# Optimization experiments

Measured on AMD Instinct MI355X. Metric: run time of the kernel, lower is better.

Reference implementation:

```python
import jax, jax.numpy as jnp
import numpy as np

DIM = 512
HEADS = 8
HD = 64
FFN = 2048
WIN = 64            # cantor_local_window; also medium-scale stride
N_LOCAL = 64        # budget 128 * 0.5
N_MED = 38          # budget 128 * 0.3
N_GLOB = 26         # remainder (ratio 0.2)
EPS = 1e-5


def _indices(S):
    # Multi-scale O(n) sampling pattern: per-query key indices [S, K].
    pos = jnp.arange(S)[:, None]
    local = jnp.clip(pos + jnp.arange(N_LOCAL) - N_LOCAL // 2, 0, S - 1)
    med_off = (jnp.arange(N_MED) - N_MED // 2) * WIN
    medium = jnp.clip(pos + med_off, 0, S - 1)
    glob = jnp.linspace(0, S - 1, N_GLOB).astype(jnp.int32)
    glob = jnp.broadcast_to(glob[None, :], (S, N_GLOB))
    return jnp.concatenate([local, medium, glob], axis=1)


def _layernorm(x, g, b):
    mu = jnp.mean(x, axis=-1, keepdims=True)
    var = jnp.mean((x - mu) ** 2, axis=-1, keepdims=True)
    return (x - mu) * jax.lax.rsqrt(var + EPS) * g + b


def _cantor_attention(x, mask, wqkv, bqkv, wo, bo):
    B, S, D = x.shape
    qkv = x @ wqkv + bqkv                      # [B,S,3D]
    q, k, v = jnp.split(qkv, 3, axis=-1)
    heads = lambda t: t.reshape(B, S, HEADS, HD).transpose(0, 2, 1, 3)
    q, k, v = heads(q), heads(k), heads(v)     # [B,H,S,hd]
    idx = _indices(S)                          # [S,K]
    k_g = k[:, :, idx, :]                      # [B,H,S,K,hd]
    v_g = v[:, :, idx, :]
    scores = jnp.einsum('bhsd,bhskd->bhsk', q, k_g) / np.sqrt(HD).astype(np.float32)
    m_g = mask[:, idx]                         # [B,S,K]
    scores = jnp.where(m_g[:, None, :, :], scores, jnp.finfo(scores.dtype).min)
    attn = jax.nn.softmax(scores, axis=-1)
    out = jnp.einsum('bhsk,bhskd->bhsd', attn, v_g)
    out = out.transpose(0, 2, 1, 3).reshape(B, S, D)
    return out @ wo + bo


def setup_inputs() -> dict:
    key = jax.random.key(0)
    ks = jax.random.split(key, 8)
    s = lambda fan: 1.0 / np.sqrt(fan)
    return {
        'x': jax.random.normal(ks[0], (1, 2048, DIM), jnp.float32),
        'attention_mask': jnp.ones((1, 2048), jnp.bool_),
        'ln1_g': jnp.ones((DIM,), jnp.float32),
        'ln1_b': jnp.zeros((DIM,), jnp.float32),
        'ln2_g': jnp.ones((DIM,), jnp.float32),
        'ln2_b': jnp.zeros((DIM,), jnp.float32),
        'wqkv': jax.random.normal(ks[1], (DIM, 3 * DIM), jnp.float32) * s(DIM),
        'bqkv': jnp.zeros((3 * DIM,), jnp.float32),
        'wo': jax.random.normal(ks[2], (DIM, DIM), jnp.float32) * s(DIM),
        'bo': jnp.zeros((DIM,), jnp.float32),
        'w1': jax.random.normal(ks[3], (DIM, FFN), jnp.float32) * s(DIM),
        'b1': jnp.zeros((FFN,), jnp.float32),
        'w2': jax.random.normal(ks[4], (FFN, DIM), jnp.float32) * s(FFN),
        'b2': jnp.zeros((DIM,), jnp.float32),
    }


def reference(x, attention_mask, ln1_g, ln1_b, ln2_g, ln2_b,
              wqkv, bqkv, wo, bo, w1, b1, w2, b2):
    # pre-norm transformer block with Cantor O(n) attention (eval mode, dropout=0)
    attn_out = _cantor_attention(_layernorm(x, ln1_g, ln1_b), attention_mask,
                                 wqkv, bqkv, wo, bo)
    x = x + attn_out
    h = _layernorm(x, ln2_g, ln2_b)
    h = jax.nn.gelu(h @ w1 + b1, approximate=False) @ w2 + b2
    return x + h
```

## Files before the change

### kernel.cpp

```cpp
#include <hip/hip_runtime.h>
#include <math.h>

typedef float f32x4 __attribute__((ext_vector_type(4)));
typedef short s16x8 __attribute__((ext_vector_type(8)));
typedef unsigned short u16x8 __attribute__((ext_vector_type(8)));
typedef unsigned short ushort_t;
typedef unsigned int uint_t;

#define D_MODEL 512
#define N_HEADS 8
#define HEAD_D  64
#define D_FFN   2048

__device__ __forceinline__ float bf2f(unsigned short u) {
  union { unsigned int i; float f; } c; c.i = ((unsigned int)u) << 16; return c.f;
}
__device__ __forceinline__ unsigned short f2bf(float f) {
  union { float f; unsigned int i; } c; c.f = f;
  unsigned int x = c.i;
  return (unsigned short)((x + 0x7FFFu + ((x >> 16) & 1u)) >> 16);
}
__device__ __forceinline__ float ldx(const void* p, size_t i, int f) {
  return f ? ((const float*)p)[i] : bf2f(((const ushort_t*)p)[i]);
}

struct DetectArgs { const void* p[14]; int n[14]; };

__global__ __launch_bounds__(256)
void detect_all(DetectArgs a, int* __restrict__ flags) {
  __shared__ int cnt[2];
  const int b = blockIdx.x;
  const int t = threadIdx.x;
  if (b == 1) { if (t == 0) flags[1] = 0; return; }
  if (t == 0) { cnt[0] = 0; cnt[1] = 0; }
  __syncthreads();
  const int n_u32 = a.n[b] >> 1;
  const int sample = n_u32 < 256 ? n_u32 : 256;
  if (t < sample) {
    uint_t u = ((const uint_t*)a.p[b])[t];
    if (u != 0u) {
      atomicAdd(&cnt[0], 1);
      int e = (u >> 7) & 0xFF;
      if (e >= 0x70 && e <= 0x83) atomicAdd(&cnt[1], 1);
    }
  }
  __syncthreads();
  if (t == 0) flags[b] = (cnt[0] >= 32 && cnt[1] * 4 <= cnt[0]) ? 1 : 0;
}

struct WDesc { const void* src; ushort_t* dst; int Kd, Nd, flag, tile0; };

__global__ __launch_bounds__(256)
void prep_kernel(WDesc w0, WDesc w1, WDesc w2, WDesc w3, int nconv,
                 const void* __restrict__ x, const void* __restrict__ g,
                 const void* __restrict__ b, ushort_t* __restrict__ h1,
                 const int* __restrict__ flags) {
  __shared__ ushort_t tile[32][33];
  const int blk = blockIdx.x;
  if (blk >= nconv) {
    const int fx = flags[0], fg = flags[2], fb = flags[3];
    const int row = (blk - nconv) * 4 + (threadIdx.x >> 6);
    const int lane = threadIdx.x & 63;
    float v[8], sum = 0.f, sq = 0.f;
#pragma unroll
    for (int i = 0; i < 8; ++i) {
      v[i] = ldx(x, (size_t)row * D_MODEL + lane * 8 + i, fx);
      sum += v[i]; sq += v[i] * v[i];
    }
#pragma unroll
    for (int o = 32; o > 0; o >>= 1) { sum += __shfl_xor(sum, o); sq += __shfl_xor(sq, o); }
    const float mu = sum * (1.0f / D_MODEL);
    const float var = sq * (1.0f / D_MODEL) - mu * mu;
    const float rstd = rsqrtf(var + 1e-5f);
#pragma unroll
    for (int i = 0; i < 8; ++i) {
      int c = lane * 8 + i;
      h1[(size_t)row * D_MODEL + c] =
          f2bf((v[i] - mu) * rstd * ldx(g, c, fg) + ldx(b, c, fb));
    }
    return;
  }
  WDesc d = (blk < w1.tile0) ? w0 : (blk < w2.tile0) ? w1 : (blk < w3.tile0) ? w2 : w3;
  const int lt = blk - d.tile0;
  const int tn = d.Nd / 32;
  const int bk = lt / tn, bn = lt % tn;
  const int f = flags[d.flag];
  const int tx = threadIdx.x & 31, ty = threadIdx.x >> 5;
#pragma unroll
  for (int r = 0; r < 4; ++r) {
    int k = bk * 32 + ty * 4 + r;
    tile[ty * 4 + r][tx] = f2bf(ldx(d.src, (size_t)k * d.Nd + bn * 32 + tx, f));
  }
  __syncthreads();
#pragma unroll
  for (int r = 0; r < 4; ++r) {
    int n = bn * 32 + ty * 4 + r;
    d.dst[(size_t)n * d.Kd + bk * 32 + tx] = tile[tx][ty * 4 + r];
  }
}

__global__ __launch_bounds__(256)
void ln1_kernel(const void* __restrict__ x, const void* __restrict__ g,
                const void* __restrict__ b, ushort_t* __restrict__ out,
                const int* __restrict__ flags) {
  const int fx = flags[0], fg = flags[2], fb = flags[3];
  const int row = blockIdx.x * 4 + (threadIdx.x >> 6);
  const int lane = threadIdx.x & 63;
  float v[8], sum = 0.f, sq = 0.f;
#pragma unroll
  for (int i = 0; i < 8; ++i) {
    v[i] = ldx(x, (size_t)row * D_MODEL + lane * 8 + i, fx);
    sum += v[i]; sq += v[i] * v[i];
  }
#pragma unroll
  for (int o = 32; o > 0; o >>= 1) { sum += __shfl_xor(sum, o); sq += __shfl_xor(sq, o); }
  const float mu = sum * (1.0f / D_MODEL);
  const float var = sq * (1.0f / D_MODEL) - mu * mu;
  const float rstd = rsqrtf(var + 1e-5f);
#pragma unroll
  for (int i = 0; i < 8; ++i) {
    int c = lane * 8 + i;
    out[(size_t)row * D_MODEL + c] =
        f2bf((v[i] - mu) * rstd * ldx(g, c, fg) + ldx(b, c, fb));
  }
}

__global__ __launch_bounds__(256)
void ln2_kernel(const float* __restrict__ y, const void* __restrict__ g,
                const void* __restrict__ b, ushort_t* __restrict__ out,
                const int* __restrict__ flags) {
  const int fg = flags[4], fb = flags[5];
  const int row = blockIdx.x * 4 + (threadIdx.x >> 6);
  const int lane = threadIdx.x & 63;
  float v[8], sum = 0.f, sq = 0.f;
#pragma unroll
  for (int i = 0; i < 8; ++i) {
    v[i] = y[(size_t)row * D_MODEL + lane * 8 + i];
    sum += v[i]; sq += v[i] * v[i];
  }
#pragma unroll
  for (int o = 32; o > 0; o >>= 1) { sum += __shfl_xor(sum, o); sq += __shfl_xor(sq, o); }
  const float mu = sum * (1.0f / D_MODEL);
  const float var = sq * (1.0f / D_MODEL) - mu * mu;
  const float rstd = rsqrtf(var + 1e-5f);
#pragma unroll
  for (int i = 0; i < 8; ++i) {
    int c = lane * 8 + i;
    out[(size_t)row * D_MODEL + c] =
        f2bf((v[i] - mu) * rstd * ldx(g, c, fg) + ldx(b, c, fb));
  }
}

template <int BM, int BN, int EPI>
__global__ __launch_bounds__(256)
void gemm_bt(const ushort_t* __restrict__ A, int lda,
             const ushort_t* __restrict__ BT, int ldb, int K,
             const void* __restrict__ bias, int bias_off,
             const void* __restrict__ res,
             float* __restrict__ yacc,
             ushort_t* __restrict__ out_bf, int ldo,
             const int* __restrict__ flags, int ibias, int ires, int addb) {
  constexpr int BK = 64;
  constexpr int FM = BM / 32, FN = BN / 32;
  constexpr int AG = BM / 32, BG = BN / 32;
  __shared__ __attribute__((aligned(16))) ushort_t As[2][BM][64];
  __shared__ __attribute__((aligned(16))) ushort_t Bs[2][BN][64];

  const int t = threadIdx.x;
  const int lane = t & 63, wave = t >> 6;
  const int wm = wave >> 1, wn = wave & 1;
  const int q = lane >> 4, lm = lane & 15;
  const int m0 = blockIdx.y * BM, n0 = blockIdx.x * BN;
  const int srow = t >> 3, sslot = t & 7;
  const int wslot = (sslot ^ (srow & 7)) * 8;
  const int xorg = lm & 7;

  f32x4 acc[FM][FN];
#pragma unroll
  for (int i = 0; i < FM; ++i)
#pragma unroll
    for (int j = 0; j < FN; ++j) acc[i][j] = (f32x4)(0.0f);

  const int fbias = flags[ibias];
  int fres = 0;
  if constexpr (EPI == 2 || EPI == 4) fres = flags[ires];
  float bbp[FN];
#pragma unroll
  for (int j = 0; j < FN; ++j) {
    if (EPI <= 2 || addb)
      bbp[j] = ldx(bias, bias_off + n0 + wn * (BN / 2) + j * 16 + lm, fbias);
    else bbp[j] = 0.0f;
  }
  float pre[FM][FN][4];
  if constexpr (EPI == 2 || EPI == 4) {
#pragma unroll
    for (int i = 0; i < FM; ++i)
#pragma unroll
      for (int j = 0; j < FN; ++j) {
        const int colg = n0 + wn * (BN / 2) + j * 16 + lm;
#pragma unroll
        for (int r = 0; r < 4; ++r) {
          const int rowg = m0 + wm * (BM / 2) + i * 16 + q * 4 + r;
          const size_t off = (size_t)rowg * ldo + colg;
          if constexpr (EPI == 2) pre[i][j][r] = ldx(res, off, fres);
          else                    pre[i][j][r] = yacc[off];
        }
      }
  }

  u16x8 av[AG], bv[BG];

  auto gload = [&](int k0) {
#pragma unroll
    for (int r = 0; r < AG; ++r)
      av[r] = *(const u16x8*)(A + (size_t)(m0 + r * 32 + srow) * lda + k0 + sslot * 8);
#pragma unroll
    for (int r = 0; r < BG; ++r)
      bv[r] = *(const u16x8*)(BT + (size_t)(n0 + r * 32 + srow) * ldb + k0 + sslot * 8);
  };
  auto swrite = [&](int buf) {
#pragma unroll
    for (int r = 0; r < AG; ++r) *(u16x8*)&As[buf][r * 32 + srow][wslot] = av[r];
#pragma unroll
    for (int r = 0; r < BG; ++r) *(u16x8*)&Bs[buf][r * 32 + srow][wslot] = bv[r];
  };
  auto frag_mfma = [&](int buf, int kh) {
    s16x8 af[FM], bf[FN];
    const int rcol = ((kh * 4 + q) ^ xorg) * 8;
#pragma unroll
    for (int i = 0; i < FM; ++i)
      af[i] = *(const s16x8*)&As[buf][wm * (BM / 2) + i * 16 + lm][rcol];
#pragma unroll
    for (int j = 0; j < FN; ++j)
      bf[j] = *(const s16x8*)&Bs[buf][wn * (BN / 2) + j * 16 + lm][rcol];
#pragma unroll
    for (int i = 0; i < FM; ++i)
#pragma unroll
      for (int j = 0; j < FN; ++j)
        acc[i][j] = __builtin_amdgcn_mfma_f32_16x16x32_bf16(af[i], bf[j], acc[i][j], 0, 0, 0);
  };

  const int NT = K / BK;
  gload(0);
  swrite(0);
  __syncthreads();
  gload(BK);
  int buf = 0;
  for (int kt = 1; kt < NT; ++kt) {
    swrite(buf ^ 1);
    if (kt + 1 < NT) gload((kt + 1) * BK);
    frag_mfma(buf, 0);
    frag_mfma(buf, 1);
    __syncthreads();
    buf ^= 1;
  }
  frag_mfma(buf, 0);
  frag_mfma(buf, 1);

#pragma unroll
  for (int i = 0; i < FM; ++i) {
#pragma unroll
    for (int j = 0; j < FN; ++j) {
      const int colg = n0 + wn * (BN / 2) + j * 16 + lm;
      const float bb = bbp[j];
#pragma unroll
      for (int r = 0; r < 4; ++r) {
        const int rowg = m0 + wm * (BM / 2) + i * 16 + q * 4 + r;
        float v = acc[i][j][r] + bb;
        const size_t off = (size_t)rowg * ldo + colg;
        if constexpr (EPI == 0) {
          out_bf[off] = f2bf(v);
        } else if constexpr (EPI == 1) {
          out_bf[off] = f2bf(0.5f * v * (1.0f + erff(v * 0.70710678f)));
        } else if constexpr (EPI == 2) {
          yacc[off] = v + pre[i][j][r];
        } else if constexpr (EPI == 3) {
          yacc[off] += v;
        } else {
          float fin = pre[i][j][r] + v;
          if (fres) ((float*)(void*)out_bf)[off] = fin;
          else      out_bf[off] = f2bf(fin);
        }
      }
    }
  }
}

template <int BM, int BN, int EPI>
__global__ __launch_bounds__(256)
void gemm_nn(const ushort_t* __restrict__ A, int lda, int K,
             const void* __restrict__ B, int ldb, int brow0, int bcol0,
             const void* __restrict__ bias, int bias_off,
             const void* __restrict__ res,
             float* __restrict__ yacc,
             ushort_t* __restrict__ out_bf, int ldo,
             const int* __restrict__ flags, int iB, int ibias, int ires, int addb) {
  constexpr int BK = 32;
  constexpr int FM = BM / 32, FN = BN / 32;
  __shared__ __attribute__((aligned(16))) ushort_t As[BM][40];
  __shared__ ushort_t Bs[BK][BN + 2];
  const int t = threadIdx.x;
  const int lane = t & 63, wave = t >> 6;
  const int wm = wave >> 1, wn = wave & 1;
  const int m0 = blockIdx.y * BM, n0 = blockIdx.x * BN;
  const int fB = flags[iB], fbias = flags[ibias];
  f32x4 acc[FM][FN];
#pragma unroll
  for (int i = 0; i < FM; ++i)
#pragma unroll
    for (int j = 0; j < FN; ++j) acc[i][j] = (f32x4)(0.0f);
  const int q = lane >> 4, lm = lane & 15;
  const int arow_s = t >> 2, aslot = t & 3;
  for (int k0 = 0; k0 < K; k0 += BK) {
    __syncthreads();
#pragma unroll
    for (int r = 0; r < BM / 64; ++r) {
      int row = r * 64 + arow_s;
      *(u16x8*)&As[row][aslot * 8] =
          *(const u16x8*)(A + (size_t)(m0 + row) * lda + k0 + aslot * 8);
    }
#pragma unroll
    for (int e = 0; e < (BK * BN) / 256; ++e) {
      int id = e * 256 + t;
      int k = id / BN, n = id % BN;
      Bs[k][n] = f2bf(ldx(B, (size_t)(brow0 + k0 + k) * ldb + bcol0 + n0 + n, fB));
    }
    __syncthreads();
    s16x8 af[FM], bf[FN];
#pragma unroll
    for (int i = 0; i < FM; ++i)
      af[i] = *(const s16x8*)&As[wm * (BM / 2) + i * 16 + lm][q * 8];
#pragma unroll
    for (int j = 0; j < FN; ++j) {
      int nl = wn * (BN / 2) + j * 16 + lm;
      u16x8 tmp;
#pragma unroll
      for (int f = 0; f < 8; ++f) tmp[f] = Bs[q * 8 + f][nl];
      bf[j] = __builtin_bit_cast(s16x8, tmp);
    }
#pragma unroll
    for (int i = 0; i < FM; ++i)
#pragma unroll
      for (int j = 0; j < FN; ++j)
        acc[i][j] = __builtin_amdgcn_mfma_f32_16x16x32_bf16(af[i], bf[j], acc[i][j], 0, 0, 0);
  }
#pragma unroll
  for (int i = 0; i < FM; ++i) {
#pragma unroll
    for (int j = 0; j < FN; ++j) {
      const int col = wn * (BN / 2) + j * 16 + lm;
      float bb = 0.0f;
      if (EPI != 3 || addb) bb = ldx(bias, bias_off + n0 + col, fbias);
#pragma unroll
      for (int r = 0; r < 4; ++r) {
        const int rowg = m0 + wm * (BM / 2) + i * 16 + q * 4 + r;
        float v = acc[i][j][r] + bb;
        if constexpr (EPI == 0) {
          out_bf[(size_t)rowg * ldo + n0 + col] = f2bf(v);
        } else if constexpr (EPI == 1) {
          out_bf[(size_t)rowg * ldo + n0 + col] =
              f2bf(0.5f * v * (1.0f + erff(v * 0.70710678f)));
        } else if constexpr (EPI == 2) {
          const size_t off = (size_t)rowg * D_MODEL + n0 + col;
          yacc[off] = v + ldx(res, off, flags[ires]);
        } else {
          const size_t off = (size_t)rowg * D_MODEL + n0 + col;
          yacc[off] += v;
        }
      }
    }
  }
}

__device__ __forceinline__ int key_index(int s, int j, int S) {
  int p;
  if (j < 64)       p = s + j - 32;
  else if (j < 102) p = s + (j - 83) * 64;
  else              p = ((j - 102) * (S - 1)) / 25;
  return min(max(p, 0), S - 1);
}

__global__ __launch_bounds__(256, 4)
void attn_kernel(const ushort_t* __restrict__ qkv, ushort_t* __restrict__ out, int S) {
  const int wave = threadIdx.x >> 6, lane = threadIdx.x & 63;
  const int nb = gridDim.x;
  int bid = blockIdx.x;
  if ((nb & 7) == 0) bid = (bid & 7) * (nb >> 3) + (bid >> 3);
  const int pair = bid * 4 + wave;
  const int h = pair / S;
  const int s = pair - h * S;
  const int g = lane >> 3, d8 = (lane & 7) * 8;

  int koff[16];
#pragma unroll
  for (int r = 0; r < 16; ++r)
    koff[r] = key_index(s, r * 8 + g, S) * (3 * D_MODEL);

  u16x8 qv8 = *(const u16x8*)(qkv + (size_t)s * (3 * D_MODEL) + h * HEAD_D + d8);
  float qf[8];
#pragma unroll
  for (int e = 0; e < 8; ++e) qf[e] = bf2f(qv8[e]);

  const ushort_t* kbase = qkv + D_MODEL + h * HEAD_D + d8;
  float pr[16];
  {
    u16x8 kv[8];
#pragma unroll
    for (int r = 0; r < 8; ++r) kv[r] = *(const u16x8*)(kbase + koff[r]);
#pragma unroll
    for (int r = 0; r < 16; ++r) {
      u16x8 cur = kv[r & 7];
      if (r < 8) kv[r & 7] = *(const u16x8*)(kbase + koff[r + 8]);
      float d = 0.f;
#pragma unroll
      for (int e = 0; e < 8; ++e) d += qf[e] * bf2f(cur[e]);
      d += __shfl_xor(d, 1);
      d += __shfl_xor(d, 2);
      d += __shfl_xor(d, 4);
      pr[r] = d * 0.125f;
    }
  }

  float mx = pr[0];
#pragma unroll
  for (int r = 1; r < 16; ++r) mx = fmaxf(mx, pr[r]);
#pragma unroll
  for (int m = 8; m <= 32; m <<= 1) mx = fmaxf(mx, __shfl_xor(mx, m));
  float sm = 0.f;
#pragma unroll
  for (int r = 0; r < 16; ++r) { pr[r] = __expf(pr[r] - mx); sm += pr[r]; }
#pragma unroll
  for (int m = 8; m <= 32; m <<= 1) sm += __shfl_xor(sm, m);
  const float inv = 1.0f / sm;

  const ushort_t* vbase = qkv + 2 * D_MODEL + h * HEAD_D + d8;
  float oacc[8];
#pragma unroll
  for (int e = 0; e < 8; ++e) oacc[e] = 0.f;
  {
    u16x8 vv[8];
#pragma unroll
    for (int r = 0; r < 8; ++r) vv[r] = *(const u16x8*)(vbase + koff[r]);
#pragma unroll
    for (int r = 0; r < 16; ++r) {
      u16x8 cv = vv[r & 7];
      float cp = pr[r] * inv;
      if (r < 8) vv[r & 7] = *(const u16x8*)(vbase + koff[r + 8]);
#pragma unroll
      for (int e = 0; e < 8; ++e) oacc[e] += cp * bf2f(cv[e]);
    }
  }
#pragma unroll
  for (int m = 8; m <= 32; m <<= 1)
#pragma unroll
    for (int e = 0; e < 8; ++e) oacc[e] += __shfl_xor(oacc[e], m);

  if (lane < 8) {
    u16x8 ov;
#pragma unroll
    for (int e = 0; e < 8; ++e) ov[e] = f2bf(oacc[e]);
    *(u16x8*)(out + (size_t)s * D_MODEL + h * HEAD_D + d8) = ov;
  }
}

__global__ __launch_bounds__(256)
void convert_kernel(const float* __restrict__ y, void* __restrict__ out,
                    const int* __restrict__ flags, int n) {
  const int fout = flags[0];
  int i = blockIdx.x * 256 + threadIdx.x;
  if (i < n) {
    float v = y[i];
    if (fout) ((float*)out)[i] = v;
    else      ((ushort_t*)out)[i] = f2bf(v);
  }
}

extern "C" void kernel_launch(void* const* d_in, const int* in_sizes, int n_in,
                              void* d_out, int out_size, void* d_ws, size_t ws_size,
                              hipStream_t stream) {
  const int S = in_sizes[0] / D_MODEL;
  const size_t sD = (size_t)S * D_MODEL;
  char* ws = (char*)d_ws;

  DetectArgs da;
  for (int i = 0; i < 14; ++i) { da.p[i] = d_in[i]; da.n[i] = in_sizes[i]; }

  ushort_t* h1    = (ushort_t*)d_out;
  ushort_t* attnb = (ushort_t*)d_out;
  ushort_t* h2    = (ushort_t*)d_out;

  const size_t MB = 1024 * 1024;
  if (ws_size >= 12 * MB + 64) {
    const int P  = (ws_size >= 20 * MB) ? 1 : 2;
    const int Nc = D_FFN / P;
    char* wbase = ws + (P == 1 ? 12 : 6) * MB;

    ushort_t* qkv   = (ushort_t*)ws;
    float*    y     = (float*)ws;
    ushort_t* gbuf  = (ushort_t*)(ws + 4 * MB);
    ushort_t* wqkvT = (ushort_t*)wbase;
    ushort_t* woT   = (ushort_t*)(wbase + 1 * MB + 512 * 1024);
    ushort_t* w1T   = (ushort_t*)(wbase + 2 * MB);
    ushort_t* w2T   = (ushort_t*)(wbase + 4 * MB);
    int*      flags = (int*)(wbase + 6 * MB);

    detect_all<<<14, 256, 0, stream>>>(da, flags);

    WDesc dq  = { d_in[6],  wqkvT, D_MODEL, 3 * D_MODEL, 6,  0 };
    WDesc dwo = { d_in[8],  woT,   D_MODEL, D_MODEL,     8,  768 };
    WDesc dw1 = { d_in[10], w1T,   D_MODEL, D_FFN,       10, 1024 };
    WDesc dw2 = { d_in[12], w2T,   D_FFN,   D_MODEL,     12, 2048 };

    prep_kernel<<<3072 + S / 4, 256, 0, stream>>>(
        dq, dwo, dw1, dw2, 3072, d_in[0], d_in[2], d_in[3], h1, flags);

    gemm_bt<32, 64, 0><<<dim3(24, S / 32), 256, 0, stream>>>(
        h1, D_MODEL, wqkvT, D_MODEL, D_MODEL, d_in[7], 0,
        nullptr, nullptr, qkv, 3 * D_MODEL, flags, 7, 0, 1);

    attn_kernel<<<(S * N_HEADS) / 4, 256, 0, stream>>>(qkv, attnb, S);

    gemm_bt<32, 32, 2><<<dim3(16, S / 32), 256, 0, stream>>>(
        attnb, D_MODEL, woT, D_MODEL, D_MODEL, d_in[9], 0,
        d_in[0], y, nullptr, D_MODEL, flags, 9, 0, 1);

    ln2_kernel<<<S / 4, 256, 0, stream>>>(y, d_in[4], d_in[5], h2, flags);

    if (P == 1) {
      gemm_bt<32, 64, 1><<<dim3(D_FFN / 64, S / 32), 256, 0, stream>>>(
          h2, D_MODEL, w1T, D_MODEL, D_MODEL,
          d_in[11], 0, nullptr, nullptr, gbuf, D_FFN, flags, 11, 0, 1);
      gemm_bt<32, 32, 4><<<dim3(16, S / 32), 256, 0, stream>>>(
          gbuf, D_FFN, w2T, D_FFN, D_FFN, d_in[13], 0,
          nullptr, y, (ushort_t*)d_out, D_MODEL, flags, 13, 0, 1);
    } else {
      gemm_bt<32, 64, 1><<<dim3(Nc / 64, S / 32), 256, 0, stream>>>(
          h2, D_MODEL, w1T, D_MODEL, D_MODEL,
          d_in[11], 0, nullptr, nullptr, gbuf, Nc, flags, 11, 0, 1);
      gemm_bt<32, 32, 3><<<dim3(16, S / 32), 256, 0, stream>>>(
          gbuf, Nc, w2T, D_FFN, Nc, d_in[13], 0,
          nullptr, y, nullptr, D_MODEL, flags, 13, 0, 1);
      gemm_bt<32, 64, 1><<<dim3(Nc / 64, S / 32), 256, 0, stream>>>(
          h2, D_MODEL, w1T + (size_t)Nc * D_MODEL, D_MODEL, D_MODEL,
          d_in[11], Nc, nullptr, nullptr, gbuf, Nc, flags, 11, 0, 1);
      gemm_bt<32, 32, 4><<<dim3(16, S / 32), 256, 0, stream>>>(
          gbuf, Nc, w2T + (size_t)Nc, D_FFN, Nc, d_in[13], 0,
          nullptr, y, (ushort_t*)d_out, D_MODEL, flags, 13, 0, 0);
    }
  } else {
    int P;
    if      (ws_size >= 12ull * MB + 4096) P = 1;
    else if (ws_size >=  8ull * MB + 4096) P = 2;
    else                                   P = 4;
    const int Nc = D_FFN / P;
    const size_t gbuf_bytes = (size_t)S * Nc * 2;
    const size_t qkv_bytes  = 3 * sD * 2;
    const size_t fo = 4ull * sD + gbuf_bytes;
    const size_t flags_pos = (qkv_bytes > fo ? qkv_bytes : fo);

    ushort_t* qkv  = (ushort_t*)ws;
    float*    y    = (float*)ws;
    ushort_t* gbuf = (ushort_t*)(ws + 4 * sD);
    int*      flags = (int*)(ws + flags_pos);

    detect_all<<<14, 256, 0, stream>>>(da, flags);
    ln1_kernel<<<S / 4, 256, 0, stream>>>(d_in[0], d_in[2], d_in[3], h1, flags);
    gemm_nn<128, 128, 0><<<dim3((3 * D_MODEL) / 128, S / 128), 256, 0, stream>>>(
        h1, D_MODEL, D_MODEL, d_in[6], 3 * D_MODEL, 0, 0, d_in[7], 0,
        nullptr, nullptr, qkv, 3 * D_MODEL, flags, 6, 7, 0, 1);
    attn_kernel<<<(S * N_HEADS) / 4, 256, 0, stream>>>(qkv, attnb, S);
    gemm_nn<64, 64, 2><<<dim3(D_MODEL / 64, S / 64), 256, 0, stream>>>(
        attnb, D_MODEL, D_MODEL, d_in[8], D_MODEL, 0, 0, d_in[9], 0,
        d_in[0], y, nullptr, D_MODEL, flags, 8, 9, 0, 1);
    ln2_kernel<<<S / 4, 256, 0, stream>>>(y, d_in[4], d_in[5], h2, flags);
    for (int p = 0; p < P; ++p) {
      if (Nc >= 1024) {
        gemm_nn<128, 128, 1><<<dim3(Nc / 128, S / 128), 256, 0, stream>>>(
            h2, D_MODEL, D_MODEL, d_in[10], D_FFN, 0, p * Nc, d_in[11], p * Nc,
            nullptr, nullptr, gbuf, Nc, flags, 10, 11, 0, 1);
      } else {
        gemm_nn<64, 64, 1><<<dim3(Nc / 64, S / 64), 256, 0, stream>>>(
            h2, D_MODEL, D_MODEL, d_in[10], D_FFN, 0, p * Nc, d_in[11], p * Nc,
            nullptr, nullptr, gbuf, Nc, flags, 10, 11, 0, 1);
      }
      gemm_nn<64, 64, 3><<<dim3(D_MODEL / 64, S / 64), 256, 0, stream>>>(
          gbuf, Nc, Nc, d_in[12], D_MODEL, p * Nc, 0, d_in[13], 0,
          nullptr, y, nullptr, D_MODEL, flags, 12, 13, 0, p == 0 ? 1 : 0);
    }
    convert_kernel<<<(int)((sD + 255) / 256), 256, 0, stream>>>(y, d_out, flags, (int)sD);
  }
}
```

Before: 181.0 us.

## Fuse LayerNorm2 into out-projection GEMM via last-block-per-row-panel counter

```diff
diff --git a/kernel.cpp b/kernel.cpp
--- a/kernel.cpp
+++ b/kernel.cpp
@@ -27,25 +27,29 @@
 struct DetectArgs { const void* p[14]; int n[14]; };
 
 __global__ __launch_bounds__(256)
-void detect_all(DetectArgs a, int* __restrict__ flags) {
-  __shared__ int cnt[2];
+void detect_all(DetectArgs a, int* __restrict__ flags, int* __restrict__ cnt) {
+  __shared__ int scnt[2];
   const int b = blockIdx.x;
   const int t = threadIdx.x;
-  if (b == 1) { if (t == 0) flags[1] = 0; return; }
-  if (t == 0) { cnt[0] = 0; cnt[1] = 0; }
+  if (b == 1) {
+    if (t == 0) flags[1] = 0;
+    if (cnt && t < 64) cnt[t] = 0;
+    return;
+  }
+  if (t == 0) { scnt[0] = 0; scnt[1] = 0; }
   __syncthreads();
   const int n_u32 = a.n[b] >> 1;
   const int sample = n_u32 < 256 ? n_u32 : 256;
   if (t < sample) {
     uint_t u = ((const uint_t*)a.p[b])[t];
     if (u != 0u) {
-      atomicAdd(&cnt[0], 1);
+      atomicAdd(&scnt[0], 1);
       int e = (u >> 7) & 0xFF;
-      if (e >= 0x70 && e <= 0x83) atomicAdd(&cnt[1], 1);
+      if (e >= 0x70 && e <= 0x83) atomicAdd(&scnt[1], 1);
     }
   }
   __syncthreads();
-  if (t == 0) flags[b] = (cnt[0] >= 32 && cnt[1] * 4 <= cnt[0]) ? 1 : 0;
+  if (t == 0) flags[b] = (scnt[0] >= 32 && scnt[1] * 4 <= scnt[0]) ? 1 : 0;
 }
 
 struct WDesc { const void* src; ushort_t* dst; int Kd, Nd, flag, tile0; };
@@ -151,7 +155,7 @@
   }
 }
 
-template <int BM, int BN, int EPI>
+template <int BM, int BN, int EPI, int LN2F>
 __global__ __launch_bounds__(256)
 void gemm_bt(const ushort_t* __restrict__ A, int lda,
              const ushort_t* __restrict__ BT, int ldb, int K,
@@ -159,12 +163,15 @@
              const void* __restrict__ res,
              float* __restrict__ yacc,
              ushort_t* __restrict__ out_bf, int ldo,
-             const int* __restrict__ flags, int ibias, int ires, int addb) {
+             const int* __restrict__ flags, int ibias, int ires, int addb,
+             const void* __restrict__ g2, const void* __restrict__ b2,
+             ushort_t* __restrict__ h2out, int* __restrict__ panel_cnt) {
   constexpr int BK = 64;
   constexpr int FM = BM / 32, FN = BN / 32;
   constexpr int AG = BM / 32, BG = BN / 32;
   __shared__ __attribute__((aligned(16))) ushort_t As[2][BM][64];
   __shared__ __attribute__((aligned(16))) ushort_t Bs[2][BN][64];
+  __shared__ int s_last;
 
   const int t = threadIdx.x;
   const int lane = t & 63, wave = t >> 6;
@@ -280,6 +287,40 @@
           float fin = pre[i][j][r] + v;
           if (fres) ((float*)(void*)out_bf)[off] = fin;
           else      out_bf[off] = f2bf(fin);
+        }
+      }
+    }
+  }
+
+  if constexpr (EPI == 2 && LN2F) {
+    __threadfence();
+    if (t == 0) {
+      int old = __hip_atomic_fetch_add(panel_cnt + blockIdx.y, 1,
+                                       __ATOMIC_ACQ_REL, __HIP_MEMORY_SCOPE_AGENT);
+      s_last = (old == (int)gridDim.x - 1) ? 1 : 0;
+    }
+    __syncthreads();
+    if (s_last) {
+      __threadfence();
+      const int fg = flags[4], fb = flags[5];
+      const int rbase = m0 + wave * 8;
+      for (int rr = 0; rr < 8; ++rr) {
+        const int row = rbase + rr;
+        float v[8], sum = 0.f, sq = 0.f;
+#pragma unroll
+        for (int i2 = 0; i2 < 8; ++i2) {
+          v[i2] = yacc[(size_t)row * ldo + lane * 8 + i2];
+          sum += v[i2]; sq += v[i2] * v[i2];
+        }
+#pragma unroll
+        for (int o = 32; o > 0; o >>= 1) { sum += __shfl_xor(sum, o); sq += __shfl_xor(sq, o); }
+        const float mu = sum * (1.0f / D_MODEL);
+        const float rstd = rsqrtf(sq * (1.0f / D_MODEL) - mu * mu + 1e-5f);
+#pragma unroll
+        for (int i2 = 0; i2 < 8; ++i2) {
+          int c = lane * 8 + i2;
+          h2out[(size_t)row * D_MODEL + c] =
+              f2bf((v[i2] - mu) * rstd * ldx(g2, c, fg) + ldx(b2, c, fb));
         }
       }
     }
@@ -503,8 +544,9 @@
     ushort_t* w1T   = (ushort_t*)(wbase + 2 * MB);
     ushort_t* w2T   = (ushort_t*)(wbase + 4 * MB);
     int*      flags = (int*)(wbase + 6 * MB);
-
-    detect_all<<<14, 256, 0, stream>>>(da, flags);
+    int*      cnt   = (int*)(wbase + 6 * MB + 1024);
+
+    detect_all<<<14, 256, 0, stream>>>(da, flags, cnt);
 
     WDesc dq  = { d_in[6],  wqkvT, D_MODEL, 3 * D_MODEL, 6,  0 };
     WDesc dwo = { d_in[8],  woT,   D_MODEL, D_MODEL,     8,  768 };
@@ -514,38 +556,44 @@
     prep_kernel<<<3072 + S / 4, 256, 0, stream>>>(
         dq, dwo, dw1, dw2, 3072, d_in[0], d_in[2], d_in[3], h1, flags);
 
-    gemm_bt<32, 64, 0><<<dim3(24, S / 32), 256, 0, stream>>>(
+    gemm_bt<32, 64, 0, 0><<<dim3(24, S / 32), 256, 0, stream>>>(
         h1, D_MODEL, wqkvT, D_MODEL, D_MODEL, d_in[7], 0,
-        nullptr, nullptr, qkv, 3 * D_MODEL, flags, 7, 0, 1);
+        nullptr, nullptr, qkv, 3 * D_MODEL, flags, 7, 0, 1,
+        nullptr, nullptr, nullptr, nullptr);
 
     attn_kernel<<<(S * N_HEADS) / 4, 256, 0, stream>>>(qkv, attnb, S);
 
-    gemm_bt<32, 32, 2><<<dim3(16, S / 32), 256, 0, stream>>>(
+    gemm_bt<32, 32, 2, 1><<<dim3(16, S / 32), 256, 0, stream>>>(
         attnb, D_MODEL, woT, D_MODEL, D_MODEL, d_in[9], 0,
-        d_in[0], y, nullptr, D_MODEL, flags, 9, 0, 1);
-
-    ln2_kernel<<<S / 4, 256, 0, stream>>>(y, d_in[4], d_in[5], h2, flags);
+        d_in[0], y, nullptr, D_MODEL, flags, 9, 0, 1,
+        d_in[4], d_in[5], h2, cnt);
 
     if (P == 1) {
-      gemm_bt<32, 64, 1><<<dim3(D_FFN / 64, S / 32), 256, 0, stream>>>(
+      gemm_bt<32, 64, 1, 0><<<dim3(D_FFN / 64, S / 32), 256, 0, stream>>>(
           h2, D_MODEL, w1T, D_MODEL, D_MODEL,
-          d_in[11], 0, nullptr, nullptr, gbuf, D_FFN, flags, 11, 0, 1);
-      gemm_bt<32, 32, 4><<<dim3(16, S / 32), 256, 0, stream>>>(
+          d_in[11], 0, nullptr, nullptr, gbuf, D_FFN, flags, 11, 0, 1,
+          nullptr, nullptr, nullptr, nullptr);
+      gemm_bt<32, 32, 4, 0><<<dim3(16, S / 32), 256, 0, stream>>>(
           gbuf, D_FFN, w2T, D_FFN, D_FFN, d_in[13], 0,
-          nullptr, y, (ushort_t*)d_out, D_MODEL, flags, 13, 0, 1);
+          nullptr, y, (ushort_t*)d_out, D_MODEL, flags, 13, 0, 1,
+          nullptr, nullptr, nullptr, nullptr);
     } else {
-      gemm_bt<32, 64, 1><<<dim3(Nc / 64, S / 32), 256, 0, stream>>>(
+      gemm_bt<32, 64, 1, 0><<<dim3(Nc / 64, S / 32), 256, 0, stream>>>(
           h2, D_MODEL, w1T, D_MODEL, D_MODEL,
-          d_in[11], 0, nullptr, nullptr, gbuf, Nc, flags, 11, 0, 1);
-      gemm_bt<32, 32, 3><<<dim3(16, S / 32), 256, 0, stream>>>(
+          d_in[11], 0, nullptr, nullptr, gbuf, Nc, flags, 11, 0, 1,
+          nullptr, nullptr, nullptr, nullptr);
+      gemm_bt<32, 32, 3, 0><<<dim3(16, S / 32), 256, 0, stream>>>(
           gbuf, Nc, w2T, D_FFN, Nc, d_in[13], 0,
-          nullptr, y, nullptr, D_MODEL, flags, 13, 0, 1);
-      gemm_bt<32, 64, 1><<<dim3(Nc / 64, S / 32), 256, 0, stream>>>(
+          nullptr, y, nullptr, D_MODEL, flags, 13, 0, 1,
+          nullptr, nullptr, nullptr, nullptr);
+      gemm_bt<32, 64, 1, 0><<<dim3(Nc / 64, S / 32), 256, 0, stream>>>(
           h2, D_MODEL, w1T + (size_t)Nc * D_MODEL, D_MODEL, D_MODEL,
-          d_in[11], Nc, nullptr, nullptr, gbuf, Nc, flags, 11, 0, 1);
-      gemm_bt<32, 32, 4><<<dim3(16, S / 32), 256, 0, stream>>>(
+          d_in[11], Nc, nullptr, nullptr, gbuf, Nc, flags, 11, 0, 1,
+          nullptr, nullptr, nullptr, nullptr);
+      gemm_bt<32, 32, 4, 0><<<dim3(16, S / 32), 256, 0, stream>>>(
           gbuf, Nc, w2T + (size_t)Nc, D_FFN, Nc, d_in[13], 0,
-          nullptr, y, (ushort_t*)d_out, D_MODEL, flags, 13, 0, 0);
+          nullptr, y, (ushort_t*)d_out, D_MODEL, flags, 13, 0, 0,
+          nullptr, nullptr, nullptr, nullptr);
     }
   } else {
     int P;
@@ -563,7 +611,7 @@
     ushort_t* gbuf = (ushort_t*)(ws + 4 * sD);
     int*      flags = (int*)(ws + flags_pos);
 
-    detect_all<<<14, 256, 0, stream>>>(da, flags);
+    detect_all<<<14, 256, 0, stream>>>(da, flags, nullptr);
     ln1_kernel<<<S / 4, 256, 0, stream>>>(d_in[0], d_in[2], d_in[3], h1, flags);
     gemm_nn<128, 128, 0><<<dim3((3 * D_MODEL) / 128, S / 128), 256, 0, stream>>>(
         h1, D_MODEL, D_MODEL, d_in[6], 3 * D_MODEL, 0, 0, d_in[7], 0,
```

New measurement: 345.7 us. 91.0% more time.
